# Performance work log

Measured on AMD Instinct MI355X. Metric: run time of the kernel, lower is better.

Reference implementation:

```python
import jax, jax.numpy as jnp
import numpy as np

N_VERTS = 40962  # icosphere level-6 vertex count
K_RING = 19      # 2-ring filter size


def setup_inputs() -> dict:
    key = jax.random.key(0)
    k1, k2, k3, k4 = jax.random.split(key, 4)
    B, C_in, C_out = 4, 64, 64
    x = jax.random.normal(k1, (B, C_in, N_VERTS), dtype=jnp.float32)
    neigh_orders = jax.random.randint(k2, (N_VERTS, K_RING), 0, N_VERTS, dtype=jnp.int32)
    # nn.Linear(19*in_feats, out_feats): weight [C_out, 19*C_in], bias [C_out]
    fan_in = K_RING * C_in
    bound = 1.0 / np.sqrt(fan_in)
    W = jax.random.uniform(k3, (C_out, fan_in), dtype=jnp.float32, minval=-bound, maxval=bound)
    b = jax.random.uniform(k4, (C_out,), dtype=jnp.float32, minval=-bound, maxval=bound)
    return {"x": x, "neigh_orders": neigh_orders, "W": W, "b": b}


def reference(x, neigh_orders, W, b):
    # x: [B, C_in, N] -> [B, N, C_in]
    xt = jnp.transpose(x, (0, 2, 1))
    B, N, C = xt.shape
    # gather 19-ring neighbors: [B, N, 19, C_in]
    gathered = xt[:, neigh_orders, :]
    # im2col-style flatten: [B, N, 19*C_in]
    mat = gathered.reshape(B, N, K_RING * C)
    # Linear: mat @ W.T + b -> [B, N, C_out]
    out = jnp.einsum('bnk,ok->bno', mat, W) + b
    # back to [B, C_out, N]
    return jnp.transpose(out, (0, 2, 1))
```

## Files before the change

kernel.cpp:

```cpp
#include <hip/hip_runtime.h>
#include <hip/hip_bf16.h>


#define NV   40962
#define KR   19
#define CIN  64
#define COUT 64
#define NB   4
#define NTILES 321

typedef __bf16 bf16;
typedef __bf16 bf16x8 __attribute__((ext_vector_type(8)));
typedef float  floatx4 __attribute__((ext_vector_type(4)));

#define XT_ELEMS ((size_t)NB * NV * CIN)
#define WB_OFF   ((XT_ELEMS * 2 + 255) & ~(size_t)255)
#define WS_NEED  (WB_OFF + (size_t)COUT * KR * CIN * 2)

__global__ __launch_bounds__(256) void transpose_kernel(
    const float* __restrict__ x, bf16* __restrict__ xt)
{
    __shared__ float tile[64 * 65];
    const int b  = blockIdx.y;
    const int v0 = blockIdx.x * 64;
    const int t  = threadIdx.x;

    const int vl = t & 63;
    const int c0 = t >> 6;
    const int vg = min(v0 + vl, NV - 1);
    #pragma unroll
    for (int p = 0; p < 16; ++p) {
        int c = c0 * 16 + p;
        tile[vl * 65 + c] = x[((size_t)(b * CIN + c)) * NV + vg];
    }
    __syncthreads();

    const int v = t >> 2;
    const int q = t & 3;
    if (v0 + v < NV) {
        #pragma unroll
        for (int p = 0; p < 2; ++p) {
            int chunk = q + p * 4;
            bf16x8 o;
            #pragma unroll
            for (int j = 0; j < 8; ++j)
                o[j] = (bf16)tile[v * 65 + chunk * 8 + j];
            *(bf16x8*)&xt[((size_t)(b * NV + v0 + v)) * 64 + chunk * 8] = o;
        }
    }
}

__global__ __launch_bounds__(256) void convw_kernel(
    const float* __restrict__ W, bf16* __restrict__ Wf)
{
    const int idx = blockIdx.x * 256 + threadIdx.x;
    if (idx >= KR * 8 * 64) return;
    const int lane = idx & 63;
    const int f    = (idx >> 6) & 7;
    const int ring = idx >> 9;
    const int ot   = f >> 1;
    const int kc   = f & 1;
    const int row  = ot * 16 + (lane & 15);
    const int col0 = ring * 64 + kc * 32 + (lane >> 4) * 8;
    const float* src = W + (size_t)row * (KR * CIN) + col0;
    float4 a = *(const float4*)(src);
    float4 c = *(const float4*)(src + 4);
    bf16x8 o;
    o[0] = (bf16)a.x; o[1] = (bf16)a.y; o[2] = (bf16)a.z; o[3] = (bf16)a.w;
    o[4] = (bf16)c.x; o[5] = (bf16)c.y; o[6] = (bf16)c.z; o[7] = (bf16)c.w;
    *(bf16x8*)(Wf + (size_t)idx * 8) = o;
}

__global__ __launch_bounds__(256, 3) void conv_kernel(
    const int*   __restrict__ neigh,
    const bf16*  __restrict__ xt,
    const bf16*  __restrict__ Wf,
    const float* __restrict__ bias,
    float*       __restrict__ out)
{
    const int i    = blockIdx.x;
    const int b    = (i & 7) >> 1;
    const int tile = (i >> 3) * 2 + (i & 1);
    if (tile >= NTILES) return;

    const int t    = threadIdx.x;
    const int wv   = t >> 6;
    const int lane = t & 63;
    const int l15  = lane & 15;
    const int g    = lane >> 4;

    const int n0 = tile * 128 + wv * 32;

    int nn[2], ib[2];
    #pragma unroll
    for (int s = 0; s < 2; ++s) {
        nn[s] = n0 + s * 16 + l15;
        ib[s] = min(nn[s], NV - 1) * KR;
    }

    const bf16* xb = xt + (((size_t)b * NV) << 6) + g * 8;
    const bf16* wb = Wf + lane * 8;

    floatx4 acc[2][4];
    #pragma unroll
    for (int s = 0; s < 2; ++s)
        #pragma unroll
        for (int o = 0; o < 4; ++o)
            acc[s][o] = (floatx4){0.f, 0.f, 0.f, 0.f};

    int icur[2], inxt[2];
    #pragma unroll
    for (int s = 0; s < 2; ++s) {
        icur[s] = neigh[ib[s] + 0];
        inxt[s] = neigh[ib[s] + 1];
    }
    bf16x8 xf[2][2], wf[8];
    #pragma unroll
    for (int s = 0; s < 2; ++s) {
        int v = ((unsigned)icur[s] < (unsigned)NV) ? icur[s] : 0;
        const bf16* p = xb + ((size_t)v << 6);
        xf[s][0] = *(const bf16x8*)(p);
        xf[s][1] = *(const bf16x8*)(p + 32);
    }
    #pragma unroll
    for (int f = 0; f < 8; ++f)
        wf[f] = *(const bf16x8*)(wb + f * 512);

    #pragma unroll
    for (int r = 0; r < KR; ++r) {
        int i2[2];
        bf16x8 xg[2][2], wg[8];

        if (r + 2 < KR) {
            #pragma unroll
            for (int s = 0; s < 2; ++s)
                i2[s] = neigh[ib[s] + r + 2];
        }
        if (r + 1 < KR) {
            #pragma unroll
            for (int s = 0; s < 2; ++s) {
                int v = ((unsigned)inxt[s] < (unsigned)NV) ? inxt[s] : 0;
                const bf16* p = xb + ((size_t)v << 6);
                xg[s][0] = *(const bf16x8*)(p);
                xg[s][1] = *(const bf16x8*)(p + 32);
            }
            const bf16* wr = wb + (size_t)(r + 1) * 4096;
            #pragma unroll
            for (int f = 0; f < 8; ++f)
                wg[f] = *(const bf16x8*)(wr + f * 512);
        }

        __builtin_amdgcn_s_setprio(1);
        #pragma unroll
        for (int kc = 0; kc < 2; ++kc)
            #pragma unroll
            for (int ot = 0; ot < 4; ++ot)
                #pragma unroll
                for (int s = 0; s < 2; ++s)
                    acc[s][ot] = __builtin_amdgcn_mfma_f32_16x16x32_bf16(
                        wf[ot * 2 + kc], xf[s][kc], acc[s][ot], 0, 0, 0);
        __builtin_amdgcn_s_setprio(0);

        if (r + 1 < KR) {
            #pragma unroll
            for (int s = 0; s < 2; ++s) {
                xf[s][0] = xg[s][0];
                xf[s][1] = xg[s][1];
                icur[s]  = inxt[s];
            }
            #pragma unroll
            for (int f = 0; f < 8; ++f)
                wf[f] = wg[f];
        }
        if (r + 2 < KR) {
            #pragma unroll
            for (int s = 0; s < 2; ++s)
                inxt[s] = i2[s];
        }
    }

    #pragma unroll
    for (int ot = 0; ot < 4; ++ot) {
        #pragma unroll
        for (int ii = 0; ii < 4; ++ii) {
            const int o = ot * 16 + g * 4 + ii;
            const float bv = bias[o];
            #pragma unroll
            for (int s = 0; s < 2; ++s) {
                if (nn[s] < NV) {
                    out[((size_t)(b * COUT + o)) * NV + nn[s]] =
                        acc[s][ot][ii] + bv;
                }
            }
        }
    }
}

__global__ __launch_bounds__(64) void fallback_kernel(
    const int*   __restrict__ neigh,
    const float* __restrict__ x,
    const float* __restrict__ W,
    const float* __restrict__ bias,
    float*       __restrict__ out)
{
    __shared__ float xg[KR * CIN];
    const int bn = blockIdx.x;
    const int b  = bn / NV;
    const int n  = bn % NV;
    const int t  = threadIdx.x;

    for (int k = t; k < KR * CIN; k += 64) {
        int r = k / CIN, c = k - r * CIN;
        int v = neigh[n * KR + r];
        v = ((unsigned)v < (unsigned)NV) ? v : 0;
        xg[k] = x[((size_t)(b * CIN + c)) * NV + v];
    }
    __syncthreads();

    float s = bias[t];
    const float* wrow = W + (size_t)t * (KR * CIN);
    for (int k = 0; k < KR * CIN; ++k) s += xg[k] * wrow[k];
    out[((size_t)(b * COUT + t)) * NV + n] = s;
}

extern "C" void kernel_launch(void* const* d_in, const int* in_sizes, int n_in,
                              void* d_out, int out_size, void* d_ws, size_t ws_size,
                              hipStream_t stream)
{
    const float* x     = (const float*)d_in[0];
    const int*   neigh = (const int*)d_in[1];
    const float* W     = (const float*)d_in[2];
    const float* bias  = (const float*)d_in[3];
    float* out = (float*)d_out;

    if (d_ws != nullptr && ws_size >= WS_NEED) {
        bf16* xt = (bf16*)d_ws;
        bf16* Wf = (bf16*)((char*)d_ws + WB_OFF);

        dim3 tgrid((NV + 63) / 64, NB);
        transpose_kernel<<<tgrid, 256, 0, stream>>>(x, xt);
        convw_kernel<<<(KR * 8 * 64 + 255) / 256, 256, 0, stream>>>(W, Wf);

        int nblk = 8 * ((NTILES + 1) / 2);
        conv_kernel<<<nblk, 256, 0, stream>>>(neigh, xt, Wf, bias, out);
    } else {
        fallback_kernel<<<NB * NV, 64, 0, stream>>>(neigh, x, W, bias, out);
    }
}
```

Measured before the change: 179.5 us.

## Split input channels into halves with separate conv blocks and bf16 partial reduction

The transposed activations are stored as two 32-channel halves per batch, so each gathered neighbor row is 64 bytes instead of 128. The conv is split across the K dimension: one block per channel half accumulates its partial sum, half 0 writes fp32 output plus bias and half 1 writes a bf16 partial, and a separate reduce kernel adds them. Other changes are vectorised float4 loads in the transpose, nontemporal stores, and a deeper neighbor-index prefetch. This doubles the number of blocks to improve latency hiding on the gathers. In exchange it adds an extra kernel and extra output read/write traffic, and rounds half the sum to bf16, which costs some precision.

```diff
diff --git a/kernel.cpp b/kernel.cpp
--- a/kernel.cpp
+++ b/kernel.cpp
@@ -15,7 +15,10 @@
 
 #define XT_ELEMS ((size_t)NB * NV * CIN)
 #define WB_OFF   ((XT_ELEMS * 2 + 255) & ~(size_t)255)
-#define WS_NEED  (WB_OFF + (size_t)COUT * KR * CIN * 2)
+#define WF_BYTES ((size_t)COUT * KR * CIN * 2)
+#define P1_OFF   ((WB_OFF + WF_BYTES + 255) & ~(size_t)255)
+#define WS_SPLIT (P1_OFF + XT_ELEMS * 2)
+#define WS_MID   (WB_OFF + WF_BYTES)
 
 __global__ __launch_bounds__(256) void transpose_kernel(
     const float* __restrict__ x, bf16* __restrict__ xt)
@@ -25,13 +28,27 @@
     const int v0 = blockIdx.x * 64;
     const int t  = threadIdx.x;
 
-    const int vl = t & 63;
-    const int c0 = t >> 6;
-    const int vg = min(v0 + vl, NV - 1);
-    #pragma unroll
-    for (int p = 0; p < 16; ++p) {
-        int c = c0 * 16 + p;
-        tile[vl * 65 + c] = x[((size_t)(b * CIN + c)) * NV + vg];
+    if (v0 + 64 <= NV) {
+        #pragma unroll
+        for (int r = 0; r < 4; ++r) {
+            int flat = r * 256 + t;
+            int c    = flat >> 4;
+            int v4   = (flat & 15) * 4;
+            floatx4 val = *(const floatx4*)&x[((size_t)(b * CIN + c)) * NV + v0 + v4];
+            tile[(v4 + 0) * 65 + c] = val.x;
+            tile[(v4 + 1) * 65 + c] = val.y;
+            tile[(v4 + 2) * 65 + c] = val.z;
+            tile[(v4 + 3) * 65 + c] = val.w;
+        }
+    } else {
+        const int vl = t & 63;
+        const int c0 = t >> 6;
+        const int vg = min(v0 + vl, NV - 1);
+        #pragma unroll
+        for (int p = 0; p < 16; ++p) {
+            int c = c0 * 16 + p;
+            tile[vl * 65 + c] = x[((size_t)(b * CIN + c)) * NV + vg];
+        }
     }
     __syncthreads();
 
@@ -45,7 +62,9 @@
             #pragma unroll
             for (int j = 0; j < 8; ++j)
                 o[j] = (bf16)tile[v * 65 + chunk * 8 + j];
-            *(bf16x8*)&xt[((size_t)(b * NV + v0 + v)) * 64 + chunk * 8] = o;
+            int kc = chunk >> 2;
+            size_t dst = ((size_t)((b * 2 + kc) * NV + v0 + v)) * 32 + (chunk & 3) * 8;
+            __builtin_nontemporal_store(o, (bf16x8*)&xt[dst]);
         }
     }
 }
@@ -54,24 +73,175 @@
     const float* __restrict__ W, bf16* __restrict__ Wf)
 {
     const int idx = blockIdx.x * 256 + threadIdx.x;
-    if (idx >= KR * 8 * 64) return;
+    if (idx >= 2 * KR * 4 * 64) return;
     const int lane = idx & 63;
-    const int f    = (idx >> 6) & 7;
-    const int ring = idx >> 9;
-    const int ot   = f >> 1;
-    const int kc   = f & 1;
+    const int ot   = (idx >> 6) & 3;
+    const int q    = idx >> 8;
+    const int kc   = (q >= KR) ? 1 : 0;
+    const int ring = q - kc * KR;
     const int row  = ot * 16 + (lane & 15);
     const int col0 = ring * 64 + kc * 32 + (lane >> 4) * 8;
     const float* src = W + (size_t)row * (KR * CIN) + col0;
-    float4 a = *(const float4*)(src);
-    float4 c = *(const float4*)(src + 4);
+    floatx4 a = *(const floatx4*)(src);
+    floatx4 c = *(const floatx4*)(src + 4);
     bf16x8 o;
     o[0] = (bf16)a.x; o[1] = (bf16)a.y; o[2] = (bf16)a.z; o[3] = (bf16)a.w;
     o[4] = (bf16)c.x; o[5] = (bf16)c.y; o[6] = (bf16)c.z; o[7] = (bf16)c.w;
     *(bf16x8*)(Wf + (size_t)idx * 8) = o;
 }
 
-__global__ __launch_bounds__(256, 3) void conv_kernel(
+__global__ __launch_bounds__(256, 3) void conv_split_kernel(
+    const int*   __restrict__ neigh,
+    const bf16*  __restrict__ xt,
+    const bf16*  __restrict__ Wf,
+    const float* __restrict__ bias,
+    float*       __restrict__ out,
+    bf16*        __restrict__ P1)
+{
+    const int i     = blockIdx.x;
+    const int slice = i & 7;
+    const int b     = slice >> 1;
+    const int kc    = slice & 1;
+    const int tile  = i >> 3;
+
+    const int t    = threadIdx.x;
+    const int wv   = t >> 6;
+    const int lane = t & 63;
+    const int l15  = lane & 15;
+    const int g    = lane >> 4;
+
+    const int n0 = tile * 128 + wv * 32;
+    int nn[2], ib[2];
+    #pragma unroll
+    for (int s = 0; s < 2; ++s) {
+        nn[s] = n0 + s * 16 + l15;
+        ib[s] = min(nn[s], NV - 1) * KR;
+    }
+
+    const bf16* xb = xt + ((size_t)slice * NV) * 32 + g * 8;
+    const bf16* wb = Wf + (size_t)kc * (KR * 2048) + lane * 8;
+
+    floatx4 acc[2][4];
+    #pragma unroll
+    for (int s = 0; s < 2; ++s)
+        #pragma unroll
+        for (int o = 0; o < 4; ++o)
+            acc[s][o] = (floatx4){0.f, 0.f, 0.f, 0.f};
+
+    int inxt[2], i3rd[2];
+    bf16x8 xf[2], xg[2], wf[4];
+    #pragma unroll
+    for (int s = 0; s < 2; ++s) {
+        int v0i = neigh[ib[s] + 0];
+        inxt[s] = neigh[ib[s] + 1];
+        i3rd[s] = neigh[ib[s] + 2];
+        int v = ((unsigned)v0i < (unsigned)NV) ? v0i : 0;
+        xf[s] = *(const bf16x8*)(xb + (size_t)v * 32);
+    }
+    #pragma unroll
+    for (int f = 0; f < 4; ++f)
+        wf[f] = *(const bf16x8*)(wb + f * 512);
+    #pragma unroll
+    for (int s = 0; s < 2; ++s) {
+        int v = ((unsigned)inxt[s] < (unsigned)NV) ? inxt[s] : 0;
+        xg[s] = *(const bf16x8*)(xb + (size_t)v * 32);
+    }
+
+    #pragma unroll
+    for (int r = 0; r < KR; ++r) {
+        int inew[2];
+        bf16x8 wg[4], xh[2];
+
+        if (r + 3 < KR) {
+            #pragma unroll
+            for (int s = 0; s < 2; ++s)
+                inew[s] = neigh[ib[s] + r + 3];
+        }
+        if (r + 1 < KR) {
+            const bf16* wr = wb + (size_t)(r + 1) * 2048;
+            #pragma unroll
+            for (int f = 0; f < 4; ++f)
+                wg[f] = *(const bf16x8*)(wr + f * 512);
+        }
+        if (r + 2 < KR) {
+            #pragma unroll
+            for (int s = 0; s < 2; ++s) {
+                int v = ((unsigned)i3rd[s] < (unsigned)NV) ? i3rd[s] : 0;
+                xh[s] = *(const bf16x8*)(xb + (size_t)v * 32);
+            }
+        }
+
+        __builtin_amdgcn_s_setprio(1);
+        #pragma unroll
+        for (int ot = 0; ot < 4; ++ot)
+            #pragma unroll
+            for (int s = 0; s < 2; ++s)
+                acc[s][ot] = __builtin_amdgcn_mfma_f32_16x16x32_bf16(
+                    wf[ot], xf[s], acc[s][ot], 0, 0, 0);
+        __builtin_amdgcn_s_setprio(0);
+
+        if (r + 1 < KR) {
+            #pragma unroll
+            for (int s = 0; s < 2; ++s) xf[s] = xg[s];
+            #pragma unroll
+            for (int f = 0; f < 4; ++f) wf[f] = wg[f];
+        }
+        if (r + 2 < KR) {
+            #pragma unroll
+            for (int s = 0; s < 2; ++s) { xg[s] = xh[s]; inxt[s] = i3rd[s]; i3rd[s] = (r + 3 < KR) ? inew[s] : 0; }
+        }
+    }
+
+    if (kc == 0) {
+        #pragma unroll
+        for (int ot = 0; ot < 4; ++ot) {
+            #pragma unroll
+            for (int ii = 0; ii < 4; ++ii) {
+                const int o = ot * 16 + g * 4 + ii;
+                const float bv = bias[o];
+                #pragma unroll
+                for (int s = 0; s < 2; ++s) {
+                    if (nn[s] < NV)
+                        __builtin_nontemporal_store(acc[s][ot][ii] + bv,
+                            &out[((size_t)(b * COUT + o)) * NV + nn[s]]);
+                }
+            }
+        }
+    } else {
+        #pragma unroll
+        for (int ot = 0; ot < 4; ++ot) {
+            #pragma unroll
+            for (int ii = 0; ii < 4; ++ii) {
+                const int o = ot * 16 + g * 4 + ii;
+                #pragma unroll
+                for (int s = 0; s < 2; ++s) {
+                    if (nn[s] < NV)
+                        __builtin_nontemporal_store((bf16)acc[s][ot][ii],
+                            &P1[((size_t)(b * COUT + o)) * NV + nn[s]]);
+                }
+            }
+        }
+    }
+}
+
+__global__ __launch_bounds__(256) void reduce_kernel(
+    float* __restrict__ out, const bf16* __restrict__ P1)
+{
+    const size_t total8 = XT_ELEMS / 8;
+    for (size_t j = (size_t)blockIdx.x * 256 + threadIdx.x; j < total8;
+         j += (size_t)gridDim.x * 256) {
+        bf16x8 p = __builtin_nontemporal_load((const bf16x8*)P1 + j);
+        floatx4* op = (floatx4*)out + j * 2;
+        floatx4 a = __builtin_nontemporal_load(op);
+        floatx4 c = __builtin_nontemporal_load(op + 1);
+        a.x += (float)p[0]; a.y += (float)p[1]; a.z += (float)p[2]; a.w += (float)p[3];
+        c.x += (float)p[4]; c.y += (float)p[5]; c.z += (float)p[6]; c.w += (float)p[7];
+        __builtin_nontemporal_store(a, op);
+        __builtin_nontemporal_store(c, op + 1);
+    }
+}
+
+__global__ __launch_bounds__(256, 3) void conv_nosplit_kernel(
     const int*   __restrict__ neigh,
     const bf16*  __restrict__ xt,
     const bf16*  __restrict__ Wf,
@@ -90,7 +260,6 @@
     const int g    = lane >> 4;
 
     const int n0 = tile * 128 + wv * 32;
-
     int nn[2], ib[2];
     #pragma unroll
     for (int s = 0; s < 2; ++s) {
@@ -98,8 +267,9 @@
         ib[s] = min(nn[s], NV - 1) * KR;
     }
 
-    const bf16* xb = xt + (((size_t)b * NV) << 6) + g * 8;
-    const bf16* wb = Wf + lane * 8;
+    const bf16* xb0 = xt + ((size_t)(b * 2 + 0) * NV) * 32 + g * 8;
+    const bf16* xb1 = xt + ((size_t)(b * 2 + 1) * NV) * 32 + g * 8;
+    const bf16* wb  = Wf + lane * 8;
 
     floatx4 acc[2][4];
     #pragma unroll
@@ -108,46 +278,43 @@
         for (int o = 0; o < 4; ++o)
             acc[s][o] = (floatx4){0.f, 0.f, 0.f, 0.f};
 
-    int icur[2], inxt[2];
+    int inxt[2];
+    bf16x8 xf[2][2], wf[2][4];
     #pragma unroll
     for (int s = 0; s < 2; ++s) {
-        icur[s] = neigh[ib[s] + 0];
+        int v0i = neigh[ib[s] + 0];
         inxt[s] = neigh[ib[s] + 1];
-    }
-    bf16x8 xf[2][2], wf[8];
-    #pragma unroll
-    for (int s = 0; s < 2; ++s) {
-        int v = ((unsigned)icur[s] < (unsigned)NV) ? icur[s] : 0;
-        const bf16* p = xb + ((size_t)v << 6);
-        xf[s][0] = *(const bf16x8*)(p);
-        xf[s][1] = *(const bf16x8*)(p + 32);
-    }
-    #pragma unroll
-    for (int f = 0; f < 8; ++f)
-        wf[f] = *(const bf16x8*)(wb + f * 512);
+        int v = ((unsigned)v0i < (unsigned)NV) ? v0i : 0;
+        xf[s][0] = *(const bf16x8*)(xb0 + (size_t)v * 32);
+        xf[s][1] = *(const bf16x8*)(xb1 + (size_t)v * 32);
+    }
+    #pragma unroll
+    for (int kc = 0; kc < 2; ++kc)
+        #pragma unroll
+        for (int f = 0; f < 4; ++f)
+            wf[kc][f] = *(const bf16x8*)(wb + (size_t)kc * (KR * 2048) + f * 512);
 
     #pragma unroll
     for (int r = 0; r < KR; ++r) {
-        int i2[2];
-        bf16x8 xg[2][2], wg[8];
-
+        int inew[2];
+        bf16x8 wg[2][4], xg[2][2];
         if (r + 2 < KR) {
             #pragma unroll
-            for (int s = 0; s < 2; ++s)
-                i2[s] = neigh[ib[s] + r + 2];
+            for (int s = 0; s < 2; ++s) inew[s] = neigh[ib[s] + r + 2];
         }
         if (r + 1 < KR) {
+            #pragma unroll
+            for (int kc = 0; kc < 2; ++kc)
+                #pragma unroll
+                for (int f = 0; f < 4; ++f)
+                    wg[kc][f] = *(const bf16x8*)(wb + (size_t)kc * (KR * 2048)
+                                                 + (size_t)(r + 1) * 2048 + f * 512);
             #pragma unroll
             for (int s = 0; s < 2; ++s) {
                 int v = ((unsigned)inxt[s] < (unsigned)NV) ? inxt[s] : 0;
-                const bf16* p = xb + ((size_t)v << 6);
-                xg[s][0] = *(const bf16x8*)(p);
-                xg[s][1] = *(const bf16x8*)(p + 32);
-            }
-            const bf16* wr = wb + (size_t)(r + 1) * 4096;
-            #pragma unroll
-            for (int f = 0; f < 8; ++f)
-                wg[f] = *(const bf16x8*)(wr + f * 512);
+                xg[s][0] = *(const bf16x8*)(xb0 + (size_t)v * 32);
+                xg[s][1] = *(const bf16x8*)(xb1 + (size_t)v * 32);
+            }
         }
 
         __builtin_amdgcn_s_setprio(1);
@@ -158,7 +325,7 @@
                 #pragma unroll
                 for (int s = 0; s < 2; ++s)
                     acc[s][ot] = __builtin_amdgcn_mfma_f32_16x16x32_bf16(
-                        wf[ot * 2 + kc], xf[s][kc], acc[s][ot], 0, 0, 0);
+                        wf[kc][ot], xf[s][kc], acc[s][ot], 0, 0, 0);
         __builtin_amdgcn_s_setprio(0);
 
         if (r + 1 < KR) {
@@ -166,16 +333,13 @@
             for (int s = 0; s < 2; ++s) {
                 xf[s][0] = xg[s][0];
                 xf[s][1] = xg[s][1];
-                icur[s]  = inxt[s];
-            }
-            #pragma unroll
-            for (int f = 0; f < 8; ++f)
-                wf[f] = wg[f];
-        }
-        if (r + 2 < KR) {
-            #pragma unroll
-            for (int s = 0; s < 2; ++s)
-                inxt[s] = i2[s];
+                inxt[s]  = (r + 2 < KR) ? inew[s] : 0;
+            }
+            #pragma unroll
+            for (int kc = 0; kc < 2; ++kc)
+                #pragma unroll
+                for (int f = 0; f < 4; ++f)
+                    wf[kc][f] = wg[kc][f];
         }
     }
 
@@ -187,10 +351,8 @@
             const float bv = bias[o];
             #pragma unroll
             for (int s = 0; s < 2; ++s) {
-                if (nn[s] < NV) {
-                    out[((size_t)(b * COUT + o)) * NV + nn[s]] =
-                        acc[s][ot][ii] + bv;
-                }
+                if (nn[s] < NV)
+                    out[((size_t)(b * COUT + o)) * NV + nn[s]] = acc[s][ot][ii] + bv;
             }
         }
     }
@@ -233,16 +395,23 @@
     const float* bias  = (const float*)d_in[3];
     float* out = (float*)d_out;
 
-    if (d_ws != nullptr && ws_size >= WS_NEED) {
+    if (d_ws != nullptr && ws_size >= WS_MID) {
         bf16* xt = (bf16*)d_ws;
         bf16* Wf = (bf16*)((char*)d_ws + WB_OFF);
 
         dim3 tgrid((NV + 63) / 64, NB);
         transpose_kernel<<<tgrid, 256, 0, stream>>>(x, xt);
-        convw_kernel<<<(KR * 8 * 64 + 255) / 256, 256, 0, stream>>>(W, Wf);
-
-        int nblk = 8 * ((NTILES + 1) / 2);
-        conv_kernel<<<nblk, 256, 0, stream>>>(neigh, xt, Wf, bias, out);
+        convw_kernel<<<(2 * KR * 4 * 64 + 255) / 256, 256, 0, stream>>>(W, Wf);
+
+        if (ws_size >= WS_SPLIT) {
+            bf16* P1 = (bf16*)((char*)d_ws + P1_OFF);
+            conv_split_kernel<<<8 * NTILES, 256, 0, stream>>>(
+                neigh, xt, Wf, bias, out, P1);
+            reduce_kernel<<<2048, 256, 0, stream>>>(out, P1);
+        } else {
+            int nblk = 8 * ((NTILES + 1) / 2);
+            conv_nosplit_kernel<<<nblk, 256, 0, stream>>>(neigh, xt, Wf, bias, out);
+        }
     } else {
         fallback_kernel<<<NB * NV, 64, 0, stream>>>(neigh, x, W, bias, out);
     }
```

Measured after the change: 193.8 us. 8.0% more time.
